# Kernel optimization log

Measured on AMD Instinct MI355X. Metric: run time of the kernel, lower is better.

Reference implementation:

```python
import jax, jax.numpy as jnp
import numpy as np

NC = 50000
NG = 2000
D = 64
NE = 1000000
NP = 500000
BN_EPS = 1e-5


def setup_inputs() -> dict:
    key = jax.random.key(0)
    ks = jax.random.split(key, 16)
    return {
        "cell_feat1": jax.random.normal(ks[0], (NC, D), jnp.float32) * 0.05,
        "cell_feat2": jax.random.normal(ks[1], (NC, D), jnp.float32) * 0.05,
        "gene_feat": jax.random.normal(ks[2], (NG, D), jnp.float32) * 0.05,
        "emb_W": jax.random.normal(ks[3], (D + 2, D), jnp.float32) * 0.05,
        "emb_b": jnp.zeros((D,), jnp.float32),
        "bn_gamma": jnp.ones((D,), jnp.float32),
        "bn_beta": jnp.zeros((D,), jnp.float32),
        "bn_mean": jnp.zeros((D,), jnp.float32),
        "bn_var": jnp.ones((D,), jnp.float32),
        "enc_src1": jax.random.randint(ks[4], (NE,), 0, NC, jnp.int32),
        "enc_dst1": jax.random.randint(ks[5], (NE,), 0, NG, jnp.int32),
        "enc_src2": jax.random.randint(ks[6], (NE,), 0, NC, jnp.int32),
        "enc_dst2": jax.random.randint(ks[7], (NE,), 0, NG, jnp.int32),
        "pos_src1": jax.random.randint(ks[8], (NP,), 0, NC, jnp.int32),
        "pos_dst1": jax.random.randint(ks[9], (NP,), 0, NG, jnp.int32),
        "pos_src2": jax.random.randint(ks[10], (NP,), 0, NC, jnp.int32),
        "pos_dst2": jax.random.randint(ks[11], (NP,), 0, NG, jnp.int32),
    }


def _inv_sqrt_deg(idx, n):
    # deg^{-1/2} per node, 0 for isolated nodes; shape (n, 1)
    deg = jax.ops.segment_sum(jnp.ones_like(idx, jnp.float32), idx, num_segments=n)
    return jnp.where(deg > 0, jax.lax.rsqrt(jnp.maximum(deg, 1.0)), 0.0)[:, None]


def reference(cell_feat1, cell_feat2, gene_feat, emb_W, emb_b,
              bn_gamma, bn_beta, bn_mean, bn_var,
              enc_src1, enc_dst1, enc_src2, enc_dst2,
              pos_src1, pos_dst1, pos_src2, pos_dst2):
    nc, ng = cell_feat1.shape[0], gene_feat.shape[0]
    # degree normalizers per relation (cj = src deg^-1/2, ci = dst deg^-1/2)
    cj_c1 = _inv_sqrt_deg(enc_src1, nc)
    ci_g1 = _inv_sqrt_deg(enc_dst1, ng)
    cj_c2 = _inv_sqrt_deg(enc_src2, nc)
    ci_g2 = _inv_sqrt_deg(enc_dst2, ng)

    def spmm(src_feats, cj, src_idx, dst_idx, ci, n_dst):
        # gather-scale-scatter-scale: ci * sum_{j in N(i)} cj_j * h_j
        msgs = (src_feats * cj)[src_idx]
        return ci * jax.ops.segment_sum(msgs, dst_idx, num_segments=n_dst)

    def layer(c1, c2, g):
        # cell -> gene (two edge types, HeteroGraphConv aggregate='mean')
        g1 = spmm(c1, cj_c1, enc_src1, enc_dst1, ci_g1, ng)
        g2 = spmm(c2, cj_c2, enc_src2, enc_dst2, ci_g2, ng)
        g_new = 0.5 * (g1 + g2)
        # gene -> cell (reverse edges; roles of ci/cj swap)
        c1_new = spmm(g, ci_g1, enc_dst1, enc_src1, cj_c1, nc)
        c2_new = spmm(g, ci_g2, enc_dst2, enc_src2, cj_c2, nc)
        return c1_new, c2_new, g_new

    w = jnp.float32(1.0 / 3.0)  # n_layers == 2 -> weights [1/3, 1/3, 1/3]
    u1, u2, ih = w * cell_feat1, w * cell_feat2, w * gene_feat
    c1, c2, g = cell_feat1, cell_feat2, gene_feat
    for _ in range(2):
        c1, c2, g = layer(c1, c2, g)
        u1 = u1 + w * c1
        u2 = u2 + w * c2
        ih = ih + w * g

    # emb_layer: Linear(d+2 -> d) on [feat | batch one-hot], BN (eval), ELU
    def emb(u, onehot):
        x = jnp.concatenate([u, jnp.broadcast_to(onehot, (u.shape[0], 2))], axis=1)
        y = x @ emb_W + emb_b
        y = bn_gamma * (y - bn_mean) * jax.lax.rsqrt(bn_var + BN_EPS) + bn_beta
        return jax.nn.elu(y)

    uf1 = emb(u1, jnp.array([1.0, 0.0], jnp.float32))
    uf2 = emb(u2, jnp.array([0.0, 1.0], jnp.float32))

    # DotDecoder: per-positive-edge dot product
    pred1 = jnp.sum(uf1[pos_src1] * ih[pos_dst1], axis=1)
    pred2 = jnp.sum(uf2[pos_src2] * ih[pos_dst2], axis=1)
    return jnp.concatenate([pred1, pred2])
```

## Files before the change

kernel.cpp:

```cpp
#include <hip/hip_runtime.h>
#include <math.h>

#define NC   50000
#define NG   2000
#define DD   64
#define NE   1000000
#define NPOS 500000
#define WTH  (1.0f/3.0f)

#define GSTRIDE 640
#define CSTRIDE 64

#define NRNGB  256
#define RNGCB  196
#define RCAP   4608
#define NRNGG  250
#define GPRG   8
#define RCAPG  4608
#define CHUNKB 4096

typedef unsigned short u16;
typedef unsigned char  u8;

__device__ __forceinline__ float bf2f(u16 u) {
    return __uint_as_float(((unsigned)u) << 16);
}
__device__ __forceinline__ u16 f2bf(float f) {
    unsigned x = __float_as_uint(f);
    return (u16)((x + 0x7FFFu + ((x >> 16) & 1u)) >> 16);
}
__device__ __forceinline__ float blo(unsigned u) { return __uint_as_float(u << 16); }
__device__ __forceinline__ float bhi(unsigned u) { return __uint_as_float(u & 0xFFFF0000u); }

__global__ __launch_bounds__(256) void k_bin2(
    const int* __restrict__ s1, const int* __restrict__ d1,
    const int* __restrict__ s2, const int* __restrict__ d2,
    int* __restrict__ rcnt_c1, int* __restrict__ rcnt_c2,
    int* __restrict__ rcnt_g1, int* __restrict__ rcnt_g2,
    unsigned* __restrict__ rbc1, unsigned* __restrict__ rbc2,
    unsigned* __restrict__ rbg1, unsigned* __restrict__ rbg2)
{
    __shared__ unsigned ed[CHUNKB];
    __shared__ unsigned hc[NRNGB], bc[NRNGB];
    __shared__ unsigned hg[NRNGG], bg[NRNGG];
    const int* src; const int* dst; int* rc; int* rg; unsigned* rbc; unsigned* rbg;
    if (blockIdx.y == 0) { src = s1; dst = d1; rc = rcnt_c1; rg = rcnt_g1; rbc = rbc1; rbg = rbg1; }
    else                 { src = s2; dst = d2; rc = rcnt_c2; rg = rcnt_g2; rbc = rbc2; rbg = rbg2; }
    int t = threadIdx.x;
    if (t < NRNGB) hc[t] = 0;
    if (t < NRNGG) hg[t] = 0;
    __syncthreads();
    int e0 = blockIdx.x * CHUNKB;
    #pragma unroll 4
    for (int i = 0; i < CHUNKB / 256; i++) {
        int e = e0 + i * 256 + t;
        unsigned pk = 0xFFFFFFFFu;
        if (e < NE) {
            int s = src[e], g = dst[e];
            pk = ((unsigned)s << 16) | (unsigned)g;
            atomicAdd(&hc[s / RNGCB], 1u);
            atomicAdd(&hg[g >> 3], 1u);
        }
        ed[i * 256 + t] = pk;
    }
    __syncthreads();
    if (t < NRNGB) { unsigned c = hc[t]; bc[t] = c ? (unsigned)atomicAdd(&rc[t], (int)c) : 0u; hc[t] = 0; }
    if (t < NRNGG) { unsigned c = hg[t]; bg[t] = c ? (unsigned)atomicAdd(&rg[t], (int)c) : 0u; hg[t] = 0; }
    __syncthreads();
    #pragma unroll 4
    for (int i = 0; i < CHUNKB / 256; i++) {
        unsigned pk = ed[i * 256 + t];
        if (pk != 0xFFFFFFFFu) {
            int s = (int)(pk >> 16), g = (int)(pk & 0xFFFFu);
            int r1 = s / RNGCB;
            unsigned p = bc[r1] + atomicAdd(&hc[r1], 1u);
            if (p < RCAP)
                rbc[(size_t)r1 * RCAP + p] = ((unsigned)(s - r1 * RNGCB) << 16) | (unsigned)g;
            int r2 = g >> 3;
            unsigned q = bg[r2] + atomicAdd(&hg[r2], 1u);
            if (q < RCAPG)
                rbg[(size_t)r2 * RCAPG + q] = ((unsigned)(g & 7) << 16) | (unsigned)s;
        }
    }
}

__global__ __launch_bounds__(256) void k_binfill(
    const int* __restrict__ rcnt1, const int* __restrict__ rcnt2,
    const unsigned* __restrict__ rbuf1, const unsigned* __restrict__ rbuf2,
    u16* __restrict__ adj_c1, u16* __restrict__ adj_c2,
    int* __restrict__ cnt_c1, int* __restrict__ cnt_c2)
{
    __shared__ u16 rows[RNGCB * CSTRIDE];
    __shared__ unsigned cur[(RNGCB + 3) / 4];
    const int* rcnt; const unsigned* rbuf; u16* adj; int* cnt;
    if (blockIdx.y == 0) { rcnt = rcnt1; rbuf = rbuf1; adj = adj_c1; cnt = cnt_c1; }
    else                 { rcnt = rcnt2; rbuf = rbuf2; adj = adj_c2; cnt = cnt_c2; }
    int t = threadIdx.x;
    int r = blockIdx.x;
    if (t < (RNGCB + 3) / 4) cur[t] = 0;
    __syncthreads();
    int n = rcnt[r]; if (n > RCAP) n = RCAP;
    const unsigned* buf = rbuf + (size_t)r * RCAP;
    for (int i = t; i < n; i += 256) {
        unsigned e = buf[i];
        unsigned cl = e >> 16;
        unsigned sh = 8u * (cl & 3u);
        unsigned old = atomicAdd(&cur[cl >> 2], 1u << sh);
        unsigned p = (old >> sh) & 0xFFu;
        if (p < CSTRIDE) rows[cl * CSTRIDE + p] = (u16)(e & 0xFFFFu);
    }
    __syncthreads();
    int lo = r * RNGCB;
    int valid = NC - lo; if (valid > RNGCB) valid = RNGCB;
    if (valid <= 0) return;
    if (t < valid) {
        unsigned p = (cur[t >> 2] >> (8u * (t & 3u))) & 0xFFu;
        cnt[lo + t] = (int)((p > CSTRIDE) ? CSTRIDE : p);
    }
    uint4* gd = (uint4*)(adj + (size_t)lo * CSTRIDE);
    const uint4* ls = (const uint4*)rows;
    for (int i = t; i < valid * (CSTRIDE / 8); i += 256) gd[i] = ls[i];
}

__global__ __launch_bounds__(256) void k_binfill_g(
    const int* __restrict__ rcnt1, const int* __restrict__ rcnt2,
    const unsigned* __restrict__ rbuf1, const unsigned* __restrict__ rbuf2,
    u16* __restrict__ adj_g1, u16* __restrict__ adj_g2,
    int* __restrict__ cnt_g1, int* __restrict__ cnt_g2)
{
    __shared__ u16 rows[GPRG * GSTRIDE];
    __shared__ unsigned cur[GPRG];
    const int* rcnt; const unsigned* rbuf; u16* adj; int* cnt;
    if (blockIdx.y == 0) { rcnt = rcnt1; rbuf = rbuf1; adj = adj_g1; cnt = cnt_g1; }
    else                 { rcnt = rcnt2; rbuf = rbuf2; adj = adj_g2; cnt = cnt_g2; }
    int t = threadIdx.x;
    int r = blockIdx.x;
    if (t < GPRG) cur[t] = 0;
    __syncthreads();
    int n = rcnt[r]; if (n > RCAPG) n = RCAPG;
    const unsigned* buf = rbuf + (size_t)r * RCAPG;
    for (int i = t; i < n; i += 256) {
        unsigned e = buf[i];
        unsigned gl = e >> 16;
        unsigned p = atomicAdd(&cur[gl], 1u);
        if (p < GSTRIDE) rows[gl * GSTRIDE + p] = (u16)(e & 0xFFFFu);
    }
    __syncthreads();
    if (t < GPRG) {
        unsigned p = cur[t];
        cnt[r * GPRG + t] = (int)((p > GSTRIDE) ? GSTRIDE : p);
    }
    uint4* gd = (uint4*)(adj + (size_t)r * GPRG * GSTRIDE);
    const uint4* ls = (const uint4*)rows;
    for (int i = t; i < GPRG * GSTRIDE / 8; i += 256) gd[i] = ls[i];
}

__global__ __launch_bounds__(256) void k_prep(
    const int* __restrict__ cnt_c1, const int* __restrict__ cnt_c2,
    const int* __restrict__ cnt_g1, const int* __restrict__ cnt_g2,
    const float* __restrict__ cell1, const float* __restrict__ cell2,
    const float* __restrict__ gfeat,
    float* __restrict__ cj_c1, float* __restrict__ cj_c2,
    float* __restrict__ ci_g1, float* __restrict__ ci_g2,
    u16* __restrict__ t1s, u16* __restrict__ t2s,
    u16* __restrict__ gf1s, u16* __restrict__ gf2s)
{
    int i = blockIdx.x * 4 + (threadIdx.x >> 6);
    int d = threadIdx.x & 63;
    if (i < NC) {
        int a = cnt_c1[i]; float j1 = (a > 0) ? 1.0f / sqrtf((float)a) : 0.0f;
        int b = cnt_c2[i]; float j2 = (b > 0) ? 1.0f / sqrtf((float)b) : 0.0f;
        if (d == 0) { cj_c1[i] = j1; cj_c2[i] = j2; }
        int idx = i * DD + d;
        t1s[idx] = f2bf(cell1[idx] * j1);
        t2s[idx] = f2bf(cell2[idx] * j2);
    }
    if (i < NG) {
        int a = cnt_g1[i]; float j1 = (a > 0) ? 1.0f / sqrtf((float)a) : 0.0f;
        int b = cnt_g2[i]; float j2 = (b > 0) ? 1.0f / sqrtf((float)b) : 0.0f;
        if (d == 0) { ci_g1[i] = j1; ci_g2[i] = j2; }
        int idx = i * DD + d;
        float g = gfeat[idx];
        gf1s[idx] = f2bf(g * j1);
        gf2s[idx] = f2bf(g * j2);
    }
}

__global__ __launch_bounds__(256) void k_c2g(
    const u16* __restrict__ src1s, const u16* __restrict__ src2s,
    const u16* __restrict__ adj_g1, const int* __restrict__ cnt_g1,
    const u16* __restrict__ adj_g2, const int* __restrict__ cnt_g2,
    const float* __restrict__ ci_g1, const float* __restrict__ ci_g2,
    u16* __restrict__ gb1s, u16* __restrict__ gb2s,
    const float* __restrict__ gfeat_init,
    float* __restrict__ ih, u16* __restrict__ ihb)
{
    __shared__ float l1[4][DD];
    __shared__ float l2[4][DD];
    int i   = blockIdx.x;
    int d   = threadIdx.x & 63;
    int grp = threadIdx.x >> 6;

    int n1 = cnt_g1[i]; if (n1 > GSTRIDE) n1 = GSTRIDE;
    const u16* a1 = adj_g1 + i * GSTRIDE;
    float acc1 = 0.f;
    int e = 0;
    for (; e + 32 <= n1; e += 32) {
        uint4 w = *(const uint4*)(a1 + e + grp * 8);
        int s0 = w.x & 0xFFFF, s1 = w.x >> 16, s2 = w.y & 0xFFFF, s3 = w.y >> 16;
        int s4 = w.z & 0xFFFF, s5 = w.z >> 16, s6 = w.w & 0xFFFF, s7 = w.w >> 16;
        float v0 = bf2f(src1s[s0 * DD + d]), v1 = bf2f(src1s[s1 * DD + d]);
        float v2 = bf2f(src1s[s2 * DD + d]), v3 = bf2f(src1s[s3 * DD + d]);
        float v4 = bf2f(src1s[s4 * DD + d]), v5 = bf2f(src1s[s5 * DD + d]);
        float v6 = bf2f(src1s[s6 * DD + d]), v7 = bf2f(src1s[s7 * DD + d]);
        acc1 += ((v0 + v1) + (v2 + v3)) + ((v4 + v5) + (v6 + v7));
    }
    for (int q = e + grp; q < n1; q += 4) acc1 += bf2f(src1s[a1[q] * DD + d]);

    int n2 = cnt_g2[i]; if (n2 > GSTRIDE) n2 = GSTRIDE;
    const u16* a2 = adj_g2 + i * GSTRIDE;
    float acc2 = 0.f;
    e = 0;
    for (; e + 32 <= n2; e += 32) {
        uint4 w = *(const uint4*)(a2 + e + grp * 8);
        int s0 = w.x & 0xFFFF, s1 = w.x >> 16, s2 = w.y & 0xFFFF, s3 = w.y >> 16;
        int s4 = w.z & 0xFFFF, s5 = w.z >> 16, s6 = w.w & 0xFFFF, s7 = w.w >> 16;
        float v0 = bf2f(src2s[s0 * DD + d]), v1 = bf2f(src2s[s1 * DD + d]);
        float v2 = bf2f(src2s[s2 * DD + d]), v3 = bf2f(src2s[s3 * DD + d]);
        float v4 = bf2f(src2s[s4 * DD + d]), v5 = bf2f(src2s[s5 * DD + d]);
        float v6 = bf2f(src2s[s6 * DD + d]), v7 = bf2f(src2s[s7 * DD + d]);
        acc2 += ((v0 + v1) + (v2 + v3)) + ((v4 + v5) + (v6 + v7));
    }
    for (int q = e + grp; q < n2; q += 4) acc2 += bf2f(src2s[a2[q] * DD + d]);

    l1[grp][d] = acc1; l2[grp][d] = acc2;
    __syncthreads();
    if (grp == 0) {
        float s1 = l1[0][d] + l1[1][d] + l1[2][d] + l1[3][d];
        float s2 = l2[0][d] + l2[1][d] + l2[2][d] + l2[3][d];
        float ci1 = ci_g1[i], ci2 = ci_g2[i];
        float gn = 0.5f * (ci1 * s1 + ci2 * s2);
        int idx = i * DD + d;
        if (gb1s) { gb1s[idx] = f2bf(gn * ci1); gb2s[idx] = f2bf(gn * ci2); }
        if (gfeat_init) ih[idx] = WTH * (gfeat_init[idx] + gn);
        else            ihb[idx] = f2bf(ih[idx] + WTH * gn);
    }
}

__global__ __launch_bounds__(256) void k_g2c(
    const u16* __restrict__ g1s, const u16* __restrict__ g2s,
    const u16* __restrict__ adj_c1, const int* __restrict__ cnt_c1,
    const u16* __restrict__ adj_c2, const int* __restrict__ cnt_c2,
    const float* __restrict__ cj_c1, const float* __restrict__ cj_c2,
    const float* __restrict__ cf1_init, const float* __restrict__ cf2_init,
    u16* __restrict__ c1bs, u16* __restrict__ c2bs,
    float* __restrict__ u1, float* __restrict__ u2)
{
    int i = blockIdx.x * 4 + (threadIdx.x >> 6);
    if (i >= NC) return;
    int d = threadIdx.x & 63;

    int n1 = cnt_c1[i]; if (n1 > CSTRIDE) n1 = CSTRIDE;
    int n2 = cnt_c2[i]; if (n2 > CSTRIDE) n2 = CSTRIDE;
    const u16* a1 = adj_c1 + (size_t)i * CSTRIDE;
    const u16* a2 = adj_c2 + (size_t)i * CSTRIDE;
    float acc1 = 0.f, acc2 = 0.f;
    int e1 = 0, e2 = 0;
    int m1 = n1 & ~3, m2 = n2 & ~3;
    int m = (m1 < m2) ? m1 : m2;
    for (; e1 < m; e1 += 4, e2 += 4) {
        uint2 w1 = *(const uint2*)(a1 + e1);
        uint2 w2 = *(const uint2*)(a2 + e2);
        int j0 = w1.x & 0xFFFF, j1 = w1.x >> 16, j2 = w1.y & 0xFFFF, j3 = w1.y >> 16;
        int k0 = w2.x & 0xFFFF, k1 = w2.x >> 16, k2 = w2.y & 0xFFFF, k3 = w2.y >> 16;
        float p0 = bf2f(g1s[j0 * DD + d]), p1 = bf2f(g1s[j1 * DD + d]);
        float p2 = bf2f(g1s[j2 * DD + d]), p3 = bf2f(g1s[j3 * DD + d]);
        float q0 = bf2f(g2s[k0 * DD + d]), q1 = bf2f(g2s[k1 * DD + d]);
        float q2 = bf2f(g2s[k2 * DD + d]), q3 = bf2f(g2s[k3 * DD + d]);
        acc1 += (p0 + p1) + (p2 + p3);
        acc2 += (q0 + q1) + (q2 + q3);
    }
    for (; e1 + 3 < n1; e1 += 4) {
        uint2 w1 = *(const uint2*)(a1 + e1);
        int j0 = w1.x & 0xFFFF, j1 = w1.x >> 16, j2 = w1.y & 0xFFFF, j3 = w1.y >> 16;
        acc1 += (bf2f(g1s[j0 * DD + d]) + bf2f(g1s[j1 * DD + d]))
              + (bf2f(g1s[j2 * DD + d]) + bf2f(g1s[j3 * DD + d]));
    }
    for (; e1 < n1; e1++) acc1 += bf2f(g1s[a1[e1] * DD + d]);
    for (; e2 + 3 < n2; e2 += 4) {
        uint2 w2 = *(const uint2*)(a2 + e2);
        int k0 = w2.x & 0xFFFF, k1 = w2.x >> 16, k2 = w2.y & 0xFFFF, k3 = w2.y >> 16;
        acc2 += (bf2f(g2s[k0 * DD + d]) + bf2f(g2s[k1 * DD + d]))
              + (bf2f(g2s[k2 * DD + d]) + bf2f(g2s[k3 * DD + d]));
    }
    for (; e2 < n2; e2++) acc2 += bf2f(g2s[a2[e2] * DD + d]);

    float jc1 = cj_c1[i];
    float jc2 = cj_c2[i];
    float c1n = jc1 * acc1;
    float c2n = jc2 * acc2;

    int idx = i * DD + d;
    u1[idx] = WTH * (cf1_init[idx] + c1n);
    u2[idx] = WTH * (cf2_init[idx] + c2n);
    c1bs[idx] = f2bf(c1n * jc1);
    c2bs[idx] = f2bf(c2n * jc2);
}

__global__ __launch_bounds__(256, 4) void k_g2c_emb(
    const u16* __restrict__ g1s, const u16* __restrict__ g2s,
    const u16* __restrict__ adj_c1, const int* __restrict__ cnt_c1,
    const u16* __restrict__ adj_c2, const int* __restrict__ cnt_c2,
    const float* __restrict__ cj_c1, const float* __restrict__ cj_c2,
    const float* __restrict__ u1, const float* __restrict__ u2,
    u16* __restrict__ uf1b, u16* __restrict__ uf2b,
    const float* __restrict__ W, const float* __restrict__ bb,
    const float* __restrict__ gam, const float* __restrict__ bet,
    const float* __restrict__ mea, const float* __restrict__ var)
{
    int d = threadIdx.x & 63;
    int wid = blockIdx.x * 4 + (threadIdx.x >> 6);
    int nw = gridDim.x * 4;

    float Wl[DD];
    #pragma unroll
    for (int k = 0; k < DD; k++) Wl[k] = W[k * DD + d];
    float inv = 1.0f / sqrtf(var[d] + 1e-5f);
    float ga = gam[d], be = bet[d], me = mea[d];
    float bias1 = bb[d] + W[DD * DD + d];
    float bias2 = bb[d] + W[(DD + 1) * DD + d];

    for (int i = wid; i < NC; i += nw) {
        int n1 = cnt_c1[i]; if (n1 > CSTRIDE) n1 = CSTRIDE;
        int n2 = cnt_c2[i]; if (n2 > CSTRIDE) n2 = CSTRIDE;
        const u16* a1 = adj_c1 + (size_t)i * CSTRIDE;
        const u16* a2 = adj_c2 + (size_t)i * CSTRIDE;
        float acc1 = 0.f, acc2 = 0.f;
        int e1 = 0, e2 = 0;
        int m1 = n1 & ~3, m2 = n2 & ~3;
        int m = (m1 < m2) ? m1 : m2;
        for (; e1 < m; e1 += 4, e2 += 4) {
            uint2 w1 = *(const uint2*)(a1 + e1);
            uint2 w2 = *(const uint2*)(a2 + e2);
            int j0 = w1.x & 0xFFFF, j1 = w1.x >> 16, j2 = w1.y & 0xFFFF, j3 = w1.y >> 16;
            int k0 = w2.x & 0xFFFF, k1 = w2.x >> 16, k2 = w2.y & 0xFFFF, k3 = w2.y >> 16;
            float p0 = bf2f(g1s[j0 * DD + d]), p1 = bf2f(g1s[j1 * DD + d]);
            float p2 = bf2f(g1s[j2 * DD + d]), p3 = bf2f(g1s[j3 * DD + d]);
            float q0 = bf2f(g2s[k0 * DD + d]), q1 = bf2f(g2s[k1 * DD + d]);
            float q2 = bf2f(g2s[k2 * DD + d]), q3 = bf2f(g2s[k3 * DD + d]);
            acc1 += (p0 + p1) + (p2 + p3);
            acc2 += (q0 + q1) + (q2 + q3);
        }
        for (; e1 + 3 < n1; e1 += 4) {
            uint2 w1 = *(const uint2*)(a1 + e1);
            int j0 = w1.x & 0xFFFF, j1 = w1.x >> 16, j2 = w1.y & 0xFFFF, j3 = w1.y >> 16;
            acc1 += (bf2f(g1s[j0 * DD + d]) + bf2f(g1s[j1 * DD + d]))
                  + (bf2f(g1s[j2 * DD + d]) + bf2f(g1s[j3 * DD + d]));
        }
        for (; e1 < n1; e1++) acc1 += bf2f(g1s[a1[e1] * DD + d]);
        for (; e2 + 3 < n2; e2 += 4) {
            uint2 w2 = *(const uint2*)(a2 + e2);
            int k0 = w2.x & 0xFFFF, k1 = w2.x >> 16, k2 = w2.y & 0xFFFF, k3 = w2.y >> 16;
            acc2 += (bf2f(g2s[k0 * DD + d]) + bf2f(g2s[k1 * DD + d]))
                  + (bf2f(g2s[k2 * DD + d]) + bf2f(g2s[k3 * DD + d]));
        }
        for (; e2 < n2; e2++) acc2 += bf2f(g2s[a2[e2] * DD + d]);

        int idx = i * DD + d;
        float x1 = u1[idx] + WTH * (cj_c1[i] * acc1);
        float x2 = u2[idx] + WTH * (cj_c2[i] * acc2);
        float y1 = bias1, y2 = bias2;
        #pragma unroll
        for (int k = 0; k < DD; k++) {
            float xa = __uint_as_float(
                (unsigned)__builtin_amdgcn_readlane(__float_as_uint(x1), k));
            float xb = __uint_as_float(
                (unsigned)__builtin_amdgcn_readlane(__float_as_uint(x2), k));
            y1 += xa * Wl[k];
            y2 += xb * Wl[k];
        }
        float t1 = ga * (y1 - me) * inv + be;
        t1 = (t1 > 0.f) ? t1 : expm1f(t1);
        float t2 = ga * (y2 - me) * inv + be;
        t2 = (t2 > 0.f) ? t2 : expm1f(t2);
        uf1b[idx] = f2bf(t1);
        uf2b[idx] = f2bf(t2);
    }
}

__global__ __launch_bounds__(256) void k_dec(
    const u16* __restrict__ uf1b, const u16* __restrict__ uf2b,
    const u16* __restrict__ ihb,
    const int* __restrict__ ps1, const int* __restrict__ pd1,
    const int* __restrict__ ps2, const int* __restrict__ pd2,
    float* __restrict__ out)
{
    int t = blockIdx.x * 256 + threadIdx.x;
    int e = t >> 3;
    int l = t & 7;
    if (e >= 2 * NPOS) return;
    const u16* uf; int s, g;
    if (e < NPOS) { uf = uf1b; s = ps1[e];        g = pd1[e];        }
    else          { uf = uf2b; s = ps2[e - NPOS]; g = pd2[e - NPOS]; }
    uint4 av = ((const uint4*)(uf + (size_t)s * DD))[l];
    uint4 cv = ((const uint4*)(ihb + (size_t)g * DD))[l];
    float acc = blo(av.x) * blo(cv.x) + bhi(av.x) * bhi(cv.x)
              + blo(av.y) * blo(cv.y) + bhi(av.y) * bhi(cv.y)
              + blo(av.z) * blo(cv.z) + bhi(av.z) * bhi(cv.z)
              + blo(av.w) * blo(cv.w) + bhi(av.w) * bhi(cv.w);
    acc += __shfl_xor(acc, 4);
    acc += __shfl_xor(acc, 2);
    acc += __shfl_xor(acc, 1);
    if (l == 0) out[e] = acc;
}

extern "C" void kernel_launch(void* const* d_in, const int* in_sizes, int n_in,
                              void* d_out, int out_size, void* d_ws, size_t ws_size,
                              hipStream_t stream)
{
    const float* cell1 = (const float*)d_in[0];
    const float* cell2 = (const float*)d_in[1];
    const float* gfeat = (const float*)d_in[2];
    const float* embW  = (const float*)d_in[3];
    const float* embB  = (const float*)d_in[4];
    const float* bng   = (const float*)d_in[5];
    const float* bnb   = (const float*)d_in[6];
    const float* bnm   = (const float*)d_in[7];
    const float* bnv   = (const float*)d_in[8];
    const int* es1 = (const int*)d_in[9];
    const int* ed1 = (const int*)d_in[10];
    const int* es2 = (const int*)d_in[11];
    const int* ed2 = (const int*)d_in[12];
    const int* ps1 = (const int*)d_in[13];
    const int* pd1 = (const int*)d_in[14];
    const int* ps2 = (const int*)d_in[15];
    const int* pd2 = (const int*)d_in[16];
    float* out = (float*)d_out;

    char* base = (char*)d_ws;
    size_t off = 0;
    auto alloc = [&](size_t bytes) -> void* {
        void* p = base + off;
        off = (off + bytes + 255) & ~(size_t)255;
        return p;
    };
    int* rcnt_c1 = (int*)alloc((size_t)NRNGB * 4);
    int* rcnt_c2 = (int*)alloc((size_t)NRNGB * 4);
    int* rcnt_g1 = (int*)alloc((size_t)NRNGG * 4);
    int* rcnt_g2 = (int*)alloc((size_t)NRNGG * 4);
    size_t cntEnd = off;
    int* cnt_c1 = (int*)alloc((size_t)NC * 4);
    int* cnt_c2 = (int*)alloc((size_t)NC * 4);
    int* cnt_g1 = (int*)alloc((size_t)NG * 4);
    int* cnt_g2 = (int*)alloc((size_t)NG * 4);
    float* u1 = (float*)alloc((size_t)NC * DD * 4);
    float* u2 = (float*)alloc((size_t)NC * DD * 4);
    unsigned* rbc1 = (unsigned*)u1;
    unsigned* rbc2 = rbc1 + (size_t)NRNGB * RCAP;
    unsigned* rbg1 = (unsigned*)u2;
    unsigned* rbg2 = rbg1 + (size_t)NRNGG * RCAPG;
    u16* adj_c1 = (u16*)alloc((size_t)NC * CSTRIDE * 2);
    u16* adj_c2 = (u16*)alloc((size_t)NC * CSTRIDE * 2);
    u16* adj_g1 = (u16*)alloc((size_t)NG * GSTRIDE * 2);
    u16* adj_g2 = (u16*)alloc((size_t)NG * GSTRIDE * 2);
    float* cj_c1 = (float*)alloc((size_t)NC * 4);
    float* cj_c2 = (float*)alloc((size_t)NC * 4);
    float* ci_g1 = (float*)alloc((size_t)NG * 4);
    float* ci_g2 = (float*)alloc((size_t)NG * 4);
    u16* t1s  = (u16*)alloc((size_t)NC * DD * 2);
    u16* t2s  = (u16*)alloc((size_t)NC * DD * 2);
    u16* c1bs = (u16*)alloc((size_t)NC * DD * 2);
    u16* c2bs = (u16*)alloc((size_t)NC * DD * 2);
    u16* gf1s = (u16*)alloc((size_t)NG * DD * 2);
    u16* gf2s = (u16*)alloc((size_t)NG * DD * 2);
    u16* gb1s = (u16*)alloc((size_t)NG * DD * 2);
    u16* gb2s = (u16*)alloc((size_t)NG * DD * 2);
    float* ih  = (float*)alloc((size_t)NG * DD * 4);
    u16*   ihb = (u16*)alloc((size_t)NG * DD * 2);
    (void)ws_size; (void)in_sizes; (void)n_in; (void)out_size;

    hipMemsetAsync(d_ws, 0, cntEnd, stream);

    dim3 gr((NE + CHUNKB - 1) / CHUNKB, 2);
    k_bin2<<<gr, 256, 0, stream>>>(es1, ed1, es2, ed2,
                                   rcnt_c1, rcnt_c2, rcnt_g1, rcnt_g2,
                                   rbc1, rbc2, rbg1, rbg2);
    dim3 gf(NRNGB, 2);
    k_binfill<<<gf, 256, 0, stream>>>(rcnt_c1, rcnt_c2, rbc1, rbc2,
                                      adj_c1, adj_c2, cnt_c1, cnt_c2);
    dim3 gg(NRNGG, 2);
    k_binfill_g<<<gg, 256, 0, stream>>>(rcnt_g1, rcnt_g2, rbg1, rbg2,
                                        adj_g1, adj_g2, cnt_g1, cnt_g2);
    k_prep<<<(NC + 3) / 4, 256, 0, stream>>>(cnt_c1, cnt_c2, cnt_g1, cnt_g2,
                                             cell1, cell2, gfeat,
                                             cj_c1, cj_c2, ci_g1, ci_g2,
                                             t1s, t2s, gf1s, gf2s);

    k_c2g<<<NG, 256, 0, stream>>>(t1s, t2s, adj_g1, cnt_g1, adj_g2, cnt_g2,
                                  ci_g1, ci_g2, gb1s, gb2s, gfeat, ih, nullptr);
    k_g2c<<<(NC + 3) / 4, 256, 0, stream>>>(gf1s, gf2s, adj_c1, cnt_c1, adj_c2, cnt_c2,
                                            cj_c1, cj_c2, cell1, cell2,
                                            c1bs, c2bs, u1, u2);
    k_c2g<<<NG, 256, 0, stream>>>(c1bs, c2bs, adj_g1, cnt_g1, adj_g2, cnt_g2,
                                  ci_g1, ci_g2, nullptr, nullptr, nullptr, ih, ihb);
    k_g2c_emb<<<2048, 256, 0, stream>>>(gb1s, gb2s, adj_c1, cnt_c1, adj_c2, cnt_c2,
                                        cj_c1, cj_c2, u1, u2, t1s, t2s,
                                        embW, embB, bng, bnb, bnm, bnv);
    k_dec<<<(2 * NPOS * 8 + 255) / 256, 256, 0, stream>>>(t1s, t2s, ihb,
                                                          ps1, pd1, ps2, pd2, out);
}
```

Measured before the change: 400.1 us.

## Fuse both gene-to-cell layers into one pass over interleaved gene features

Layer-2 gene features depend only on the first cell-to-gene pass, not on layer-1 cell features. So the layer-1 and layer-2 gene-to-cell aggregations are merged into one kernel. Both gene feature versions are stored interleaved as bf16 pairs, so a single 32-bit gather fetches both and each cell's adjacency list is walked once. This removes the separate k_g2c kernel and the fp32 u1/u2 intermediates (a write and re-read of two NC×64 float arrays). The embedding matmul also changes from readlane broadcasts against a per-thread register copy of W to an LDS-staged input times a pre-transposed W. That costs some LDS traffic and needs dedicated bin buffers that no longer alias u1/u2.

Result: slower. 462.5 us (+15.6%).

```diff
diff --git a/kernel.cpp b/kernel.cpp
--- a/kernel.cpp
+++ b/kernel.cpp
@@ -163,8 +163,15 @@
     float* __restrict__ cj_c1, float* __restrict__ cj_c2,
     float* __restrict__ ci_g1, float* __restrict__ ci_g2,
     u16* __restrict__ t1s, u16* __restrict__ t2s,
-    u16* __restrict__ gf1s, u16* __restrict__ gf2s)
-{
+    u16* __restrict__ gfb1, u16* __restrict__ gfb2,
+    const float* __restrict__ W, float* __restrict__ Wt)
+{
+    if (blockIdx.x == 0) {
+        for (int x = threadIdx.x; x < DD * DD; x += 256) {
+            int k = x >> 6, dd = x & 63;
+            Wt[dd * DD + k] = W[k * DD + dd];
+        }
+    }
     int i = blockIdx.x * 4 + (threadIdx.x >> 6);
     int d = threadIdx.x & 63;
     if (i < NC) {
@@ -181,8 +188,8 @@
         if (d == 0) { ci_g1[i] = j1; ci_g2[i] = j2; }
         int idx = i * DD + d;
         float g = gfeat[idx];
-        gf1s[idx] = f2bf(g * j1);
-        gf2s[idx] = f2bf(g * j2);
+        gfb1[2 * idx] = f2bf(g * j1);
+        gfb2[2 * idx] = f2bf(g * j2);
     }
 }
 
@@ -241,90 +248,31 @@
         float ci1 = ci_g1[i], ci2 = ci_g2[i];
         float gn = 0.5f * (ci1 * s1 + ci2 * s2);
         int idx = i * DD + d;
-        if (gb1s) { gb1s[idx] = f2bf(gn * ci1); gb2s[idx] = f2bf(gn * ci2); }
+        if (gb1s) { gb1s[2 * idx + 1] = f2bf(gn * ci1); gb2s[2 * idx + 1] = f2bf(gn * ci2); }
         if (gfeat_init) ih[idx] = WTH * (gfeat_init[idx] + gn);
         else            ihb[idx] = f2bf(ih[idx] + WTH * gn);
     }
 }
 
-__global__ __launch_bounds__(256) void k_g2c(
-    const u16* __restrict__ g1s, const u16* __restrict__ g2s,
+__global__ __launch_bounds__(256, 4) void k_g2c2_emb(
+    const u16* __restrict__ gfb1, const u16* __restrict__ gfb2,
     const u16* __restrict__ adj_c1, const int* __restrict__ cnt_c1,
     const u16* __restrict__ adj_c2, const int* __restrict__ cnt_c2,
     const float* __restrict__ cj_c1, const float* __restrict__ cj_c2,
-    const float* __restrict__ cf1_init, const float* __restrict__ cf2_init,
+    const float* __restrict__ cell1, const float* __restrict__ cell2,
     u16* __restrict__ c1bs, u16* __restrict__ c2bs,
-    float* __restrict__ u1, float* __restrict__ u2)
-{
-    int i = blockIdx.x * 4 + (threadIdx.x >> 6);
-    if (i >= NC) return;
-    int d = threadIdx.x & 63;
-
-    int n1 = cnt_c1[i]; if (n1 > CSTRIDE) n1 = CSTRIDE;
-    int n2 = cnt_c2[i]; if (n2 > CSTRIDE) n2 = CSTRIDE;
-    const u16* a1 = adj_c1 + (size_t)i * CSTRIDE;
-    const u16* a2 = adj_c2 + (size_t)i * CSTRIDE;
-    float acc1 = 0.f, acc2 = 0.f;
-    int e1 = 0, e2 = 0;
-    int m1 = n1 & ~3, m2 = n2 & ~3;
-    int m = (m1 < m2) ? m1 : m2;
-    for (; e1 < m; e1 += 4, e2 += 4) {
-        uint2 w1 = *(const uint2*)(a1 + e1);
-        uint2 w2 = *(const uint2*)(a2 + e2);
-        int j0 = w1.x & 0xFFFF, j1 = w1.x >> 16, j2 = w1.y & 0xFFFF, j3 = w1.y >> 16;
-        int k0 = w2.x & 0xFFFF, k1 = w2.x >> 16, k2 = w2.y & 0xFFFF, k3 = w2.y >> 16;
-        float p0 = bf2f(g1s[j0 * DD + d]), p1 = bf2f(g1s[j1 * DD + d]);
-        float p2 = bf2f(g1s[j2 * DD + d]), p3 = bf2f(g1s[j3 * DD + d]);
-        float q0 = bf2f(g2s[k0 * DD + d]), q1 = bf2f(g2s[k1 * DD + d]);
-        float q2 = bf2f(g2s[k2 * DD + d]), q3 = bf2f(g2s[k3 * DD + d]);
-        acc1 += (p0 + p1) + (p2 + p3);
-        acc2 += (q0 + q1) + (q2 + q3);
-    }
-    for (; e1 + 3 < n1; e1 += 4) {
-        uint2 w1 = *(const uint2*)(a1 + e1);
-        int j0 = w1.x & 0xFFFF, j1 = w1.x >> 16, j2 = w1.y & 0xFFFF, j3 = w1.y >> 16;
-        acc1 += (bf2f(g1s[j0 * DD + d]) + bf2f(g1s[j1 * DD + d]))
-              + (bf2f(g1s[j2 * DD + d]) + bf2f(g1s[j3 * DD + d]));
-    }
-    for (; e1 < n1; e1++) acc1 += bf2f(g1s[a1[e1] * DD + d]);
-    for (; e2 + 3 < n2; e2 += 4) {
-        uint2 w2 = *(const uint2*)(a2 + e2);
-        int k0 = w2.x & 0xFFFF, k1 = w2.x >> 16, k2 = w2.y & 0xFFFF, k3 = w2.y >> 16;
-        acc2 += (bf2f(g2s[k0 * DD + d]) + bf2f(g2s[k1 * DD + d]))
-              + (bf2f(g2s[k2 * DD + d]) + bf2f(g2s[k3 * DD + d]));
-    }
-    for (; e2 < n2; e2++) acc2 += bf2f(g2s[a2[e2] * DD + d]);
-
-    float jc1 = cj_c1[i];
-    float jc2 = cj_c2[i];
-    float c1n = jc1 * acc1;
-    float c2n = jc2 * acc2;
-
-    int idx = i * DD + d;
-    u1[idx] = WTH * (cf1_init[idx] + c1n);
-    u2[idx] = WTH * (cf2_init[idx] + c2n);
-    c1bs[idx] = f2bf(c1n * jc1);
-    c2bs[idx] = f2bf(c2n * jc2);
-}
-
-__global__ __launch_bounds__(256, 4) void k_g2c_emb(
-    const u16* __restrict__ g1s, const u16* __restrict__ g2s,
-    const u16* __restrict__ adj_c1, const int* __restrict__ cnt_c1,
-    const u16* __restrict__ adj_c2, const int* __restrict__ cnt_c2,
-    const float* __restrict__ cj_c1, const float* __restrict__ cj_c2,
-    const float* __restrict__ u1, const float* __restrict__ u2,
     u16* __restrict__ uf1b, u16* __restrict__ uf2b,
-    const float* __restrict__ W, const float* __restrict__ bb,
+    const float* __restrict__ Wt, const float* __restrict__ W,
+    const float* __restrict__ bb,
     const float* __restrict__ gam, const float* __restrict__ bet,
     const float* __restrict__ mea, const float* __restrict__ var)
 {
-    int d = threadIdx.x & 63;
-    int wid = blockIdx.x * 4 + (threadIdx.x >> 6);
-    int nw = gridDim.x * 4;
-
-    float Wl[DD];
-    #pragma unroll
-    for (int k = 0; k < DD; k++) Wl[k] = W[k * DD + d];
+    __shared__ float xs[4][2 * DD];
+    int d  = threadIdx.x & 63;
+    int wv = threadIdx.x >> 6;
+    int wid = blockIdx.x * 4 + wv;
+    int nw  = gridDim.x * 4;
+
     float inv = 1.0f / sqrtf(var[d] + 1e-5f);
     float ga = gam[d], be = bet[d], me = mea[d];
     float bias1 = bb[d] + W[DD * DD + d];
@@ -335,7 +283,7 @@
         int n2 = cnt_c2[i]; if (n2 > CSTRIDE) n2 = CSTRIDE;
         const u16* a1 = adj_c1 + (size_t)i * CSTRIDE;
         const u16* a2 = adj_c2 + (size_t)i * CSTRIDE;
-        float acc1 = 0.f, acc2 = 0.f;
+        float a1A = 0.f, a1B = 0.f, a2A = 0.f, a2B = 0.f;
         int e1 = 0, e2 = 0;
         int m1 = n1 & ~3, m2 = n2 & ~3;
         int m = (m1 < m2) ? m1 : m2;
@@ -344,40 +292,67 @@
             uint2 w2 = *(const uint2*)(a2 + e2);
             int j0 = w1.x & 0xFFFF, j1 = w1.x >> 16, j2 = w1.y & 0xFFFF, j3 = w1.y >> 16;
             int k0 = w2.x & 0xFFFF, k1 = w2.x >> 16, k2 = w2.y & 0xFFFF, k3 = w2.y >> 16;
-            float p0 = bf2f(g1s[j0 * DD + d]), p1 = bf2f(g1s[j1 * DD + d]);
-            float p2 = bf2f(g1s[j2 * DD + d]), p3 = bf2f(g1s[j3 * DD + d]);
-            float q0 = bf2f(g2s[k0 * DD + d]), q1 = bf2f(g2s[k1 * DD + d]);
-            float q2 = bf2f(g2s[k2 * DD + d]), q3 = bf2f(g2s[k3 * DD + d]);
-            acc1 += (p0 + p1) + (p2 + p3);
-            acc2 += (q0 + q1) + (q2 + q3);
+            unsigned p0 = *(const unsigned*)(gfb1 + j0 * 128 + 2 * d);
+            unsigned p1 = *(const unsigned*)(gfb1 + j1 * 128 + 2 * d);
+            unsigned p2 = *(const unsigned*)(gfb1 + j2 * 128 + 2 * d);
+            unsigned p3 = *(const unsigned*)(gfb1 + j3 * 128 + 2 * d);
+            unsigned q0 = *(const unsigned*)(gfb2 + k0 * 128 + 2 * d);
+            unsigned q1 = *(const unsigned*)(gfb2 + k1 * 128 + 2 * d);
+            unsigned q2 = *(const unsigned*)(gfb2 + k2 * 128 + 2 * d);
+            unsigned q3 = *(const unsigned*)(gfb2 + k3 * 128 + 2 * d);
+            a1A += (blo(p0) + blo(p1)) + (blo(p2) + blo(p3));
+            a1B += (bhi(p0) + bhi(p1)) + (bhi(p2) + bhi(p3));
+            a2A += (blo(q0) + blo(q1)) + (blo(q2) + blo(q3));
+            a2B += (bhi(q0) + bhi(q1)) + (bhi(q2) + bhi(q3));
         }
         for (; e1 + 3 < n1; e1 += 4) {
             uint2 w1 = *(const uint2*)(a1 + e1);
             int j0 = w1.x & 0xFFFF, j1 = w1.x >> 16, j2 = w1.y & 0xFFFF, j3 = w1.y >> 16;
-            acc1 += (bf2f(g1s[j0 * DD + d]) + bf2f(g1s[j1 * DD + d]))
-                  + (bf2f(g1s[j2 * DD + d]) + bf2f(g1s[j3 * DD + d]));
-        }
-        for (; e1 < n1; e1++) acc1 += bf2f(g1s[a1[e1] * DD + d]);
+            unsigned p0 = *(const unsigned*)(gfb1 + j0 * 128 + 2 * d);
+            unsigned p1 = *(const unsigned*)(gfb1 + j1 * 128 + 2 * d);
+            unsigned p2 = *(const unsigned*)(gfb1 + j2 * 128 + 2 * d);
+            unsigned p3 = *(const unsigned*)(gfb1 + j3 * 128 + 2 * d);
+            a1A += (blo(p0) + blo(p1)) + (blo(p2) + blo(p3));
+            a1B += (bhi(p0) + bhi(p1)) + (bhi(p2) + bhi(p3));
+        }
+        for (; e1 < n1; e1++) {
+            unsigned p = *(const unsigned*)(gfb1 + a1[e1] * 128 + 2 * d);
+            a1A += blo(p); a1B += bhi(p);
+        }
         for (; e2 + 3 < n2; e2 += 4) {
             uint2 w2 = *(const uint2*)(a2 + e2);
             int k0 = w2.x & 0xFFFF, k1 = w2.x >> 16, k2 = w2.y & 0xFFFF, k3 = w2.y >> 16;
-            acc2 += (bf2f(g2s[k0 * DD + d]) + bf2f(g2s[k1 * DD + d]))
-                  + (bf2f(g2s[k2 * DD + d]) + bf2f(g2s[k3 * DD + d]));
-        }
-        for (; e2 < n2; e2++) acc2 += bf2f(g2s[a2[e2] * DD + d]);
-
+            unsigned q0 = *(const unsigned*)(gfb2 + k0 * 128 + 2 * d);
+            unsigned q1 = *(const unsigned*)(gfb2 + k1 * 128 + 2 * d);
+            unsigned q2 = *(const unsigned*)(gfb2 + k2 * 128 + 2 * d);
+            unsigned q3 = *(const unsigned*)(gfb2 + k3 * 128 + 2 * d);
+            a2A += (blo(q0) + blo(q1)) + (blo(q2) + blo(q3));
+            a2B += (bhi(q0) + bhi(q1)) + (bhi(q2) + bhi(q3));
+        }
+        for (; e2 < n2; e2++) {
+            unsigned q = *(const unsigned*)(gfb2 + a2[e2] * 128 + 2 * d);
+            a2A += blo(q); a2B += bhi(q);
+        }
+
+        float jc1 = cj_c1[i], jc2 = cj_c2[i];
+        float c1n = jc1 * a1A;
+        float c2n = jc2 * a2A;
         int idx = i * DD + d;
-        float x1 = u1[idx] + WTH * (cj_c1[i] * acc1);
-        float x2 = u2[idx] + WTH * (cj_c2[i] * acc2);
+        c1bs[idx] = f2bf(c1n * jc1);
+        c2bs[idx] = f2bf(c2n * jc2);
+        float x1 = WTH * (cell1[idx] + c1n) + WTH * (jc1 * a1B);
+        float x2 = WTH * (cell2[idx] + c2n) + WTH * (jc2 * a2B);
+
+        xs[wv][d] = x1;
+        xs[wv][DD + d] = x2;
         float y1 = bias1, y2 = bias2;
         #pragma unroll
-        for (int k = 0; k < DD; k++) {
-            float xa = __uint_as_float(
-                (unsigned)__builtin_amdgcn_readlane(__float_as_uint(x1), k));
-            float xb = __uint_as_float(
-                (unsigned)__builtin_amdgcn_readlane(__float_as_uint(x2), k));
-            y1 += xa * Wl[k];
-            y2 += xb * Wl[k];
+        for (int k = 0; k < DD; k += 4) {
+            float4 xq1 = *(const float4*)&xs[wv][k];
+            float4 xq2 = *(const float4*)&xs[wv][DD + k];
+            float4 wq  = *(const float4*)&Wt[d * DD + k];
+            y1 += xq1.x * wq.x; y1 += xq1.y * wq.y; y1 += xq1.z * wq.z; y1 += xq1.w * wq.w;
+            y2 += xq2.x * wq.x; y2 += xq2.y * wq.y; y2 += xq2.z * wq.z; y2 += xq2.w * wq.w;
         }
         float t1 = ga * (y1 - me) * inv + be;
         t1 = (t1 > 0.f) ? t1 : expm1f(t1);
@@ -453,12 +428,10 @@
     int* cnt_c2 = (int*)alloc((size_t)NC * 4);
     int* cnt_g1 = (int*)alloc((size_t)NG * 4);
     int* cnt_g2 = (int*)alloc((size_t)NG * 4);
-    float* u1 = (float*)alloc((size_t)NC * DD * 4);
-    float* u2 = (float*)alloc((size_t)NC * DD * 4);
-    unsigned* rbc1 = (unsigned*)u1;
-    unsigned* rbc2 = rbc1 + (size_t)NRNGB * RCAP;
-    unsigned* rbg1 = (unsigned*)u2;
-    unsigned* rbg2 = rbg1 + (size_t)NRNGG * RCAPG;
+    unsigned* rbc1 = (unsigned*)alloc((size_t)NRNGB * RCAP * 4);
+    unsigned* rbc2 = (unsigned*)alloc((size_t)NRNGB * RCAP * 4);
+    unsigned* rbg1 = (unsigned*)alloc((size_t)NRNGG * RCAPG * 4);
+    unsigned* rbg2 = (unsigned*)alloc((size_t)NRNGG * RCAPG * 4);
     u16* adj_c1 = (u16*)alloc((size_t)NC * CSTRIDE * 2);
     u16* adj_c2 = (u16*)alloc((size_t)NC * CSTRIDE * 2);
     u16* adj_g1 = (u16*)alloc((size_t)NG * GSTRIDE * 2);
@@ -471,12 +444,11 @@
     u16* t2s  = (u16*)alloc((size_t)NC * DD * 2);
     u16* c1bs = (u16*)alloc((size_t)NC * DD * 2);
     u16* c2bs = (u16*)alloc((size_t)NC * DD * 2);
-    u16* gf1s = (u16*)alloc((size_t)NG * DD * 2);
-    u16* gf2s = (u16*)alloc((size_t)NG * DD * 2);
-    u16* gb1s = (u16*)alloc((size_t)NG * DD * 2);
-    u16* gb2s = (u16*)alloc((size_t)NG * DD * 2);
+    u16* gfb1 = (u16*)alloc((size_t)NG * DD * 2 * 2);
+    u16* gfb2 = (u16*)alloc((size_t)NG * DD * 2 * 2);
     float* ih  = (float*)alloc((size_t)NG * DD * 4);
     u16*   ihb = (u16*)alloc((size_t)NG * DD * 2);
+    float* Wt  = (float*)alloc((size_t)DD * DD * 4);
     (void)ws_size; (void)in_sizes; (void)n_in; (void)out_size;
 
     hipMemsetAsync(d_ws, 0, cntEnd, stream);
@@ -494,18 +466,16 @@
     k_prep<<<(NC + 3) / 4, 256, 0, stream>>>(cnt_c1, cnt_c2, cnt_g1, cnt_g2,
                                              cell1, cell2, gfeat,
                                              cj_c1, cj_c2, ci_g1, ci_g2,
-                                             t1s, t2s, gf1s, gf2s);
+                                             t1s, t2s, gfb1, gfb2, embW, Wt);
 
     k_c2g<<<NG, 256, 0, stream>>>(t1s, t2s, adj_g1, cnt_g1, adj_g2, cnt_g2,
-                                  ci_g1, ci_g2, gb1s, gb2s, gfeat, ih, nullptr);
-    k_g2c<<<(NC + 3) / 4, 256, 0, stream>>>(gf1s, gf2s, adj_c1, cnt_c1, adj_c2, cnt_c2,
-                                            cj_c1, cj_c2, cell1, cell2,
-                                            c1bs, c2bs, u1, u2);
+                                  ci_g1, ci_g2, gfb1, gfb2, gfeat, ih, nullptr);
+    k_g2c2_emb<<<2048, 256, 0, stream>>>(gfb1, gfb2, adj_c1, cnt_c1, adj_c2, cnt_c2,
+                                         cj_c1, cj_c2, cell1, cell2,
+                                         c1bs, c2bs, t1s, t2s,
+                                         Wt, embW, embB, bng, bnb, bnm, bnv);
     k_c2g<<<NG, 256, 0, stream>>>(c1bs, c2bs, adj_g1, cnt_g1, adj_g2, cnt_g2,
                                   ci_g1, ci_g2, nullptr, nullptr, nullptr, ih, ihb);
-    k_g2c_emb<<<2048, 256, 0, stream>>>(gb1s, gb2s, adj_c1, cnt_c1, adj_c2, cnt_c2,
-                                        cj_c1, cj_c2, u1, u2, t1s, t2s,
-                                        embW, embB, bng, bnb, bnm, bnv);
     k_dec<<<(2 * NPOS * 8 + 255) / 256, 256, 0, stream>>>(t1s, t2s, ihb,
                                                           ps1, pd1, ps2, pd2, out);
 }
```

## Drop register-cached weights in fused gene-to-cell embedding kernel to raise occupancy

Applied to the files above, without the earlier changes.

The fused gene-to-cell plus embedding kernel no longer keeps a 64-entry column of the weight matrix in registers, and no longer broadcasts activations with readlane. Each wave now stages its x vectors in shared memory and reads a transposed copy of W (built once in the prep kernel) with float4 loads. This frees registers so the launch bound can ask for 8 blocks per CU, and the grid is doubled, aiming to hide gather latency. The cost is 16 extra vector loads of W per lane per node, served by cache, plus LDS traffic for x.

Measured after the change: 707.5 us. 76.8% more time.

```diff
diff --git a/kernel.cpp b/kernel.cpp
--- a/kernel.cpp
+++ b/kernel.cpp
@@ -163,8 +163,15 @@
     float* __restrict__ cj_c1, float* __restrict__ cj_c2,
     float* __restrict__ ci_g1, float* __restrict__ ci_g2,
     u16* __restrict__ t1s, u16* __restrict__ t2s,
-    u16* __restrict__ gf1s, u16* __restrict__ gf2s)
-{
+    u16* __restrict__ gf1s, u16* __restrict__ gf2s,
+    const float* __restrict__ W, float* __restrict__ Wt)
+{
+    if (blockIdx.x == 0) {
+        for (int x = threadIdx.x; x < DD * DD; x += 256) {
+            int k = x >> 6, dd = x & 63;
+            Wt[dd * DD + k] = W[k * DD + dd];
+        }
+    }
     int i = blockIdx.x * 4 + (threadIdx.x >> 6);
     int d = threadIdx.x & 63;
     if (i < NC) {
@@ -307,24 +314,24 @@
     c2bs[idx] = f2bf(c2n * jc2);
 }
 
-__global__ __launch_bounds__(256, 4) void k_g2c_emb(
+__global__ __launch_bounds__(256, 8) void k_g2c_emb(
     const u16* __restrict__ g1s, const u16* __restrict__ g2s,
     const u16* __restrict__ adj_c1, const int* __restrict__ cnt_c1,
     const u16* __restrict__ adj_c2, const int* __restrict__ cnt_c2,
     const float* __restrict__ cj_c1, const float* __restrict__ cj_c2,
     const float* __restrict__ u1, const float* __restrict__ u2,
     u16* __restrict__ uf1b, u16* __restrict__ uf2b,
-    const float* __restrict__ W, const float* __restrict__ bb,
+    const float* __restrict__ Wt, const float* __restrict__ W,
+    const float* __restrict__ bb,
     const float* __restrict__ gam, const float* __restrict__ bet,
     const float* __restrict__ mea, const float* __restrict__ var)
 {
-    int d = threadIdx.x & 63;
-    int wid = blockIdx.x * 4 + (threadIdx.x >> 6);
+    __shared__ float xs[4][2 * DD];
+    int d  = threadIdx.x & 63;
+    int wv = threadIdx.x >> 6;
+    int wid = blockIdx.x * 4 + wv;
     int nw = gridDim.x * 4;
 
-    float Wl[DD];
-    #pragma unroll
-    for (int k = 0; k < DD; k++) Wl[k] = W[k * DD + d];
     float inv = 1.0f / sqrtf(var[d] + 1e-5f);
     float ga = gam[d], be = bet[d], me = mea[d];
     float bias1 = bb[d] + W[DD * DD + d];
@@ -369,15 +376,17 @@
         int idx = i * DD + d;
         float x1 = u1[idx] + WTH * (cj_c1[i] * acc1);
         float x2 = u2[idx] + WTH * (cj_c2[i] * acc2);
+
+        xs[wv][d] = x1;
+        xs[wv][DD + d] = x2;
         float y1 = bias1, y2 = bias2;
         #pragma unroll
-        for (int k = 0; k < DD; k++) {
-            float xa = __uint_as_float(
-                (unsigned)__builtin_amdgcn_readlane(__float_as_uint(x1), k));
-            float xb = __uint_as_float(
-                (unsigned)__builtin_amdgcn_readlane(__float_as_uint(x2), k));
-            y1 += xa * Wl[k];
-            y2 += xb * Wl[k];
+        for (int k = 0; k < DD; k += 4) {
+            float4 xq1 = *(const float4*)&xs[wv][k];
+            float4 xq2 = *(const float4*)&xs[wv][DD + k];
+            float4 wq  = *(const float4*)&Wt[d * DD + k];
+            y1 += xq1.x * wq.x; y1 += xq1.y * wq.y; y1 += xq1.z * wq.z; y1 += xq1.w * wq.w;
+            y2 += xq2.x * wq.x; y2 += xq2.y * wq.y; y2 += xq2.z * wq.z; y2 += xq2.w * wq.w;
         }
         float t1 = ga * (y1 - me) * inv + be;
         t1 = (t1 > 0.f) ? t1 : expm1f(t1);
@@ -477,6 +486,7 @@
     u16* gb2s = (u16*)alloc((size_t)NG * DD * 2);
     float* ih  = (float*)alloc((size_t)NG * DD * 4);
     u16*   ihb = (u16*)alloc((size_t)NG * DD * 2);
+    float* Wt  = (float*)alloc((size_t)DD * DD * 4);
     (void)ws_size; (void)in_sizes; (void)n_in; (void)out_size;
 
     hipMemsetAsync(d_ws, 0, cntEnd, stream);
@@ -494,7 +504,7 @@
     k_prep<<<(NC + 3) / 4, 256, 0, stream>>>(cnt_c1, cnt_c2, cnt_g1, cnt_g2,
                                              cell1, cell2, gfeat,
                                              cj_c1, cj_c2, ci_g1, ci_g2,
-                                             t1s, t2s, gf1s, gf2s);
+                                             t1s, t2s, gf1s, gf2s, embW, Wt);
 
     k_c2g<<<NG, 256, 0, stream>>>(t1s, t2s, adj_g1, cnt_g1, adj_g2, cnt_g2,
                                   ci_g1, ci_g2, gb1s, gb2s, gfeat, ih, nullptr);
@@ -503,9 +513,9 @@
                                             c1bs, c2bs, u1, u2);
     k_c2g<<<NG, 256, 0, stream>>>(c1bs, c2bs, adj_g1, cnt_g1, adj_g2, cnt_g2,
                                   ci_g1, ci_g2, nullptr, nullptr, nullptr, ih, ihb);
-    k_g2c_emb<<<2048, 256, 0, stream>>>(gb1s, gb2s, adj_c1, cnt_c1, adj_c2, cnt_c2,
+    k_g2c_emb<<<4096, 256, 0, stream>>>(gb1s, gb2s, adj_c1, cnt_c1, adj_c2, cnt_c2,
                                         cj_c1, cj_c2, u1, u2, t1s, t2s,
-                                        embW, embB, bng, bnb, bnm, bnv);
+                                        Wt, embW, embB, bng, bnb, bnm, bnv);
     k_dec<<<(2 * NPOS * 8 + 255) / 256, 256, 0, stream>>>(t1s, t2s, ihb,
                                                           ps1, pd1, ps2, pd2, out);
 }
```
